# Kernel optimization log

Hardware: AMD Instinct MI355X
Metric: run time of the kernel (lower is better)

Reference implementation:

```python
import jax, jax.numpy as jnp
import numpy as np

N, F, D, O, E = 100000, 32, 3, 32, 1600000


def setup_inputs() -> dict:
    key = jax.random.key(0)
    k = jax.random.split(key, 7)
    x = jax.random.normal(k[0], (N, F), dtype=jnp.float32)
    edge_index = jax.random.randint(k[1], (2, E), 0, N, dtype=jnp.int64)
    pseudo = jax.random.uniform(k[2], (E, D), dtype=jnp.float32)
    # learned params (uniform init as in torch reset_parameters)
    bound = 1.0 / np.sqrt(F)
    mu = jax.random.uniform(k[3], (F, D), minval=-bound, maxval=bound, dtype=jnp.float32)
    sigma = jax.random.uniform(k[4], (F, D), minval=0.1, maxval=1.0, dtype=jnp.float32)
    W = jax.random.uniform(k[5], (O, F), minval=-bound, maxval=bound, dtype=jnp.float32)
    b = jax.random.uniform(k[6], (O,), minval=-bound, maxval=bound, dtype=jnp.float32)
    return {"x": x, "edge_index": edge_index, "pseudo": pseudo,
            "mu": mu, "sigma": sigma, "W": W, "b": b}


def reference(x, edge_index, pseudo, mu, sigma, W, b):
    row, col = edge_index[0], edge_index[1]
    # per-edge, per-channel gaussian mixture weight: (E,F)
    diff = pseudo[:, None, :] - mu[None, :, :]           # (E,F,D)
    logw = jnp.sum(-0.5 * diff ** 2 / (1e-14 + sigma[None] ** 2), axis=-1)
    gaussian = jnp.exp(logw)                              # (E,F)
    msg = x[col] * gaussian                               # gather + weight, (E,F)
    out = jax.ops.segment_sum(msg, row, num_segments=x.shape[0])  # scatter_add, (N,F)
    return out @ W.T + b                                  # linear, (N,O)
```

## Files before the change

kernel.cpp:

```cpp
#include <hip/hip_runtime.h>

#define N_NODES 100000
#define F_DIM   32
#define D_DIM   3
#define O_DIM   32
#define E_EDGES 1600000

#define CAP        32
#define SPILL_MAX  262144
#define NSTRIPES   512
#define EPS        (E_EDGES / NSTRIPES)


struct __align__(16) Spill { unsigned row, col, q01, q2; };

__global__ __launch_bounds__(256) void k_bucket(
        const int* __restrict__ ei, const float* __restrict__ pseudo,
        int* __restrict__ cnt, int* __restrict__ spillcnt,
        unsigned long long* __restrict__ rec, Spill* __restrict__ spill) {
    const int c    = blockIdx.x & 7;
    const int s    = blockIdx.x >> 3;
    const int base = s * EPS;
    const int end  = base + EPS;

    for (int e = base + threadIdx.x; e < end; e += 256) {
        const int row = ei[e];
        if (((row >> 12) & 7) != c) continue;
        const int   col = ei[E_EDGES + e];
        const float p0  = pseudo[e * 3 + 0];
        const float p1  = pseudo[e * 3 + 1];
        const float p2  = pseudo[e * 3 + 2];
        const int p = atomicAdd(&cnt[row], 1);
        if (p < CAP) {
            const unsigned q0 = min((unsigned)(p0 * 32768.f + 0.5f), 32767u);
            const unsigned q1 = min((unsigned)(p1 * 65536.f + 0.5f), 65535u);
            const unsigned q2 = min((unsigned)(p2 * 65536.f + 0.5f), 65535u);
            const unsigned lo = (unsigned)col | (q0 << 17);
            const unsigned hi = q1 | (q2 << 16);
            rec[(size_t)row * CAP + p] = ((unsigned long long)hi << 32) | lo;
        } else {
            const int t = atomicAdd(spillcnt, 1);
            if (t < SPILL_MAX) {
                Spill sp;
                sp.row = (unsigned)row;
                sp.col = (unsigned)col;
                sp.q01 = min((unsigned)(p0 * 65536.f + 0.5f), 65535u)
                       | (min((unsigned)(p1 * 65536.f + 0.5f), 65535u) << 16);
                sp.q2  = min((unsigned)(p2 * 65536.f + 0.5f), 65535u);
                spill[t] = sp;
            }
        }
    }
}

__global__ __launch_bounds__(128) void k_gather_linear(
        const float* __restrict__ x, const int* __restrict__ cnt,
        const unsigned long long* __restrict__ rec,
        const int* __restrict__ spillcnt, const Spill* __restrict__ spill,
        const float* __restrict__ mu, const float* __restrict__ sigma,
        const float* __restrict__ W, const float* __restrict__ b,
        float* __restrict__ out) {
    __shared__ float arow[2][F_DIM];

    const int lane = threadIdx.x & 63;
    const int wid  = threadIdx.x >> 6;
    const int f    = lane & 31;
    const int half = lane >> 5;
    const int n    = blockIdx.x * 2 + wid;

    const float m0 = mu[f * 3 + 0], m1 = mu[f * 3 + 1], m2 = mu[f * 3 + 2];
    const float s0 = sigma[f * 3 + 0], s1 = sigma[f * 3 + 1], s2 = sigma[f * 3 + 2];
    const float c0 = 0.5f / (1e-14f + s0 * s0);
    const float c1 = 0.5f / (1e-14f + s1 * s1);
    const float c2 = 0.5f / (1e-14f + s2 * s2);

    const int cn = cnt[n];
    const int m  = min(cn, CAP);
    const unsigned long long* rb = rec + (size_t)n * CAP;

    unsigned long long r[16];
#pragma unroll
    for (int k = 0; k < 16; ++k) {
        r[k] = rb[half + 2 * k];
    }

    float xv[16];
#pragma unroll
    for (int k = 0; k < 16; ++k) {
        const int col = min((int)((unsigned)r[k] & 0x1FFFFu), N_NODES - 1);
        xv[k] = x[(size_t)col * F_DIM + f];
    }

    float a0 = 0.f, a1 = 0.f;
#pragma unroll
    for (int k = 0; k < 16; ++k) {
        const int j = half + 2 * k;
        if (j < m) {
            const unsigned lo = (unsigned)r[k];
            const unsigned hi = (unsigned)(r[k] >> 32);
            const float d0 = (float)(lo >> 17) * (1.f / 32768.f) - m0;
            const float d1 = (float)(hi & 0xFFFFu) * (1.f / 65536.f) - m1;
            const float d2 = (float)(hi >> 16) * (1.f / 65536.f) - m2;
            const float g  = __expf(-(c0 * d0 * d0 + c1 * d1 * d1 + c2 * d2 * d2));
            if (k & 1) a1 += xv[k] * g; else a0 += xv[k] * g;
        }
    }

    if (cn > CAP && half == 0) {
        const int sn = min(*spillcnt, SPILL_MAX);
        for (int k = 0; k < sn; ++k) {
            const Spill sp = spill[k];
            if ((int)sp.row != n) continue;
            const float d0 = (float)(sp.q01 & 0xFFFFu) * (1.f / 65536.f) - m0;
            const float d1 = (float)(sp.q01 >> 16) * (1.f / 65536.f) - m1;
            const float d2 = (float)sp.q2 * (1.f / 65536.f) - m2;
            const float g  = __expf(-(c0 * d0 * d0 + c1 * d1 * d1 + c2 * d2 * d2));
            a0 += x[(size_t)sp.col * F_DIM + f] * g;
        }
    }

    float a = a0 + a1;
    a += __shfl_xor(a, 32, 64);
    if (half == 0) arow[wid][f] = a;
    __syncthreads();

    float w[16];
    const float* wrow = W + (size_t)f * F_DIM + half * 16;
#pragma unroll
    for (int q = 0; q < 4; ++q) {
        const float4 t = ((const float4*)wrow)[q];
        w[4 * q + 0] = t.x; w[4 * q + 1] = t.y;
        w[4 * q + 2] = t.z; w[4 * q + 3] = t.w;
    }
    const float* ar = &arow[wid][half * 16];
    float s = 0.f;
#pragma unroll
    for (int q = 0; q < 4; ++q) {
        const float4 v = ((const float4*)ar)[q];
        s += v.x * w[4 * q + 0] + v.y * w[4 * q + 1]
           + v.z * w[4 * q + 2] + v.w * w[4 * q + 3];
    }
    s += __shfl_xor(s, 32, 64);
    if (half == 0) out[(size_t)n * F_DIM + f] = s + b[f];
}

__global__ void gmm_edge_scatter(const float* __restrict__ x,
                                 const int*   __restrict__ edge_index,
                                 const float* __restrict__ pseudo,
                                 const float* __restrict__ mu,
                                 const float* __restrict__ sigma,
                                 float* __restrict__ acc) {
    const int f = threadIdx.x & 31;
    const float m0 = mu[f * 3 + 0], m1 = mu[f * 3 + 1], m2 = mu[f * 3 + 2];
    const float s0 = sigma[f * 3 + 0], s1 = sigma[f * 3 + 1], s2 = sigma[f * 3 + 2];
    const float c0 = 0.5f / (1e-14f + s0 * s0);
    const float c1 = 0.5f / (1e-14f + s1 * s1);
    const float c2 = 0.5f / (1e-14f + s2 * s2);
    int group   = (blockIdx.x * blockDim.x + threadIdx.x) >> 5;
    int ngroups = (gridDim.x * blockDim.x) >> 5;
    for (int e = group; e < E_EDGES; e += ngroups) {
        const int row = edge_index[e];
        const int col = edge_index[E_EDGES + e];
        const float p0 = pseudo[e * 3 + 0], p1 = pseudo[e * 3 + 1], p2 = pseudo[e * 3 + 2];
        const float d0 = p0 - m0, d1 = p1 - m1, d2 = p2 - m2;
        const float g  = __expf(-(c0 * d0 * d0 + c1 * d1 * d1 + c2 * d2 * d2));
        atomicAdd(&acc[(size_t)row * F_DIM + f], x[(size_t)col * F_DIM + f] * g);
    }
}

__global__ void gmm_linear2(const float* __restrict__ acc,
                            const float* __restrict__ W,
                            const float* __restrict__ b,
                            float* __restrict__ out) {
    const int o = threadIdx.x & 31;
    const int n = (blockIdx.x * blockDim.x + threadIdx.x) >> 5;
    if (n >= N_NODES) return;
    const float* wrow = W + (size_t)o * F_DIM;
    const float* ap   = acc + (size_t)n * F_DIM;
    float s = b[o];
#pragma unroll
    for (int q = 0; q < 8; ++q) {
        const float4 wv = ((const float4*)wrow)[q];
        const float4 av = ((const float4*)ap)[q];
        s += av.x * wv.x + av.y * wv.y + av.z * wv.z + av.w * wv.w;
    }
    out[(size_t)n * F_DIM + o] = s;
}

extern "C" void kernel_launch(void* const* d_in, const int* in_sizes, int n_in,
                              void* d_out, int out_size, void* d_ws, size_t ws_size,
                              hipStream_t stream) {
    const float* x          = (const float*)d_in[0];
    const int*   edge_index = (const int*)  d_in[1];
    const float* pseudo     = (const float*)d_in[2];
    const float* mu         = (const float*)d_in[3];
    const float* sigma      = (const float*)d_in[4];
    const float* W          = (const float*)d_in[5];
    const float* b          = (const float*)d_in[6];
    float*       out        = (float*)d_out;

    const size_t CNT_OFF    = 0;
    const size_t SPC_OFF    = (size_t)N_NODES * 4;
    const size_t ZERO_BYTES = SPC_OFF + 4;
    const size_t REC_OFF    = 409600;
    const size_t REC_BYTES  = (size_t)N_NODES * CAP * 8;
    const size_t SPILL_OFF  = REC_OFF + REC_BYTES;
    const size_t NEED       = SPILL_OFF + (size_t)SPILL_MAX * sizeof(Spill);

    if (ws_size >= NEED) {
        char* ws = (char*)d_ws;
        int*                cnt      = (int*)(ws + CNT_OFF);
        int*                spillcnt = (int*)(ws + SPC_OFF);
        unsigned long long* rec      = (unsigned long long*)(ws + REC_OFF);
        Spill*              spill    = (Spill*)(ws + SPILL_OFF);

        hipMemsetAsync(ws, 0, ZERO_BYTES, stream);
        k_bucket<<<8 * NSTRIPES, 256, 0, stream>>>(
            edge_index, pseudo, cnt, spillcnt, rec, spill);
        k_gather_linear<<<N_NODES / 2, 128, 0, stream>>>(
            x, cnt, rec, spillcnt, spill, mu, sigma, W, b, out);
    } else {
        float* acc = (float*)d_ws;
        hipMemsetAsync(acc, 0, (size_t)N_NODES * F_DIM * sizeof(float), stream);
        gmm_edge_scatter<<<4096, 256, 0, stream>>>(x, edge_index, pseudo, mu, sigma, acc);
        gmm_linear2<<<(N_NODES * 32 + 255) / 256, 256, 0, stream>>>(acc, W, b, out);
    }
}
```

Measured before the change: 274.3 us.

## Remap gather lanes to float2 feature pairs and loop only over actual edges

```diff
diff --git a/kernel.cpp b/kernel.cpp
--- a/kernel.cpp
+++ b/kernel.cpp
@@ -53,95 +53,121 @@
     }
 }
 
-__global__ __launch_bounds__(128) void k_gather_linear(
+__global__ __launch_bounds__(256) void k_gather_linear(
         const float* __restrict__ x, const int* __restrict__ cnt,
         const unsigned long long* __restrict__ rec,
         const int* __restrict__ spillcnt, const Spill* __restrict__ spill,
         const float* __restrict__ mu, const float* __restrict__ sigma,
         const float* __restrict__ W, const float* __restrict__ b,
         float* __restrict__ out) {
-    __shared__ float arow[2][F_DIM];
+    __shared__ float arow[4][F_DIM];
 
     const int lane = threadIdx.x & 63;
     const int wid  = threadIdx.x >> 6;
-    const int f    = lane & 31;
-    const int half = lane >> 5;
-    const int n    = blockIdx.x * 2 + wid;
-
-    const float m0 = mu[f * 3 + 0], m1 = mu[f * 3 + 1], m2 = mu[f * 3 + 2];
-    const float s0 = sigma[f * 3 + 0], s1 = sigma[f * 3 + 1], s2 = sigma[f * 3 + 2];
-    const float c0 = 0.5f / (1e-14f + s0 * s0);
-    const float c1 = 0.5f / (1e-14f + s1 * s1);
-    const float c2 = 0.5f / (1e-14f + s2 * s2);
+    const int fq   = lane & 15;
+    const int q    = lane >> 4;
+    const int f0   = 2 * fq;
+    const int n    = blockIdx.x * 4 + wid;
+
+    const float ma0 = mu[f0 * 3 + 0], ma1 = mu[f0 * 3 + 1], ma2 = mu[f0 * 3 + 2];
+    const float mb0 = mu[f0 * 3 + 3], mb1 = mu[f0 * 3 + 4], mb2 = mu[f0 * 3 + 5];
+    const float sa0 = sigma[f0 * 3 + 0], sa1 = sigma[f0 * 3 + 1], sa2 = sigma[f0 * 3 + 2];
+    const float sb0 = sigma[f0 * 3 + 3], sb1 = sigma[f0 * 3 + 4], sb2 = sigma[f0 * 3 + 5];
+    const float ca0 = 0.5f / (1e-14f + sa0 * sa0);
+    const float ca1 = 0.5f / (1e-14f + sa1 * sa1);
+    const float ca2 = 0.5f / (1e-14f + sa2 * sa2);
+    const float cb0 = 0.5f / (1e-14f + sb0 * sb0);
+    const float cb1 = 0.5f / (1e-14f + sb1 * sb1);
+    const float cb2 = 0.5f / (1e-14f + sb2 * sb2);
 
     const int cn = cnt[n];
     const int m  = min(cn, CAP);
     const unsigned long long* rb = rec + (size_t)n * CAP;
-
-    unsigned long long r[16];
-#pragma unroll
-    for (int k = 0; k < 16; ++k) {
-        r[k] = rb[half + 2 * k];
-    }
-
-    float xv[16];
-#pragma unroll
-    for (int k = 0; k < 16; ++k) {
-        const int col = min((int)((unsigned)r[k] & 0x1FFFFu), N_NODES - 1);
-        xv[k] = x[(size_t)col * F_DIM + f];
-    }
-
-    float a0 = 0.f, a1 = 0.f;
-#pragma unroll
-    for (int k = 0; k < 16; ++k) {
-        const int j = half + 2 * k;
-        if (j < m) {
-            const unsigned lo = (unsigned)r[k];
-            const unsigned hi = (unsigned)(r[k] >> 32);
-            const float d0 = (float)(lo >> 17) * (1.f / 32768.f) - m0;
-            const float d1 = (float)(hi & 0xFFFFu) * (1.f / 65536.f) - m1;
-            const float d2 = (float)(hi >> 16) * (1.f / 65536.f) - m2;
-            const float g  = __expf(-(c0 * d0 * d0 + c1 * d1 * d1 + c2 * d2 * d2));
-            if (k & 1) a1 += xv[k] * g; else a0 += xv[k] * g;
-        }
-    }
-
-    if (cn > CAP && half == 0) {
+    const float2* x2 = (const float2*)x;
+
+    float Ax0 = 0.f, Ay0 = 0.f, Ax1 = 0.f, Ay1 = 0.f;
+    int j = q;
+
+    for (; j + 4 < m; j += 8) {
+        const unsigned long long r0 = rb[j];
+        const unsigned long long r1 = rb[j + 4];
+        const unsigned lo0 = (unsigned)r0, hi0 = (unsigned)(r0 >> 32);
+        const unsigned lo1 = (unsigned)r1, hi1 = (unsigned)(r1 >> 32);
+        const float2 xv0 = x2[(size_t)(lo0 & 0x1FFFFu) * 16 + fq];
+        const float2 xv1 = x2[(size_t)(lo1 & 0x1FFFFu) * 16 + fq];
+        const float u00 = (float)(lo0 >> 17) * (1.f / 32768.f);
+        const float u01 = (float)(hi0 & 0xFFFFu) * (1.f / 65536.f);
+        const float u02 = (float)(hi0 >> 16) * (1.f / 65536.f);
+        const float u10 = (float)(lo1 >> 17) * (1.f / 32768.f);
+        const float u11 = (float)(hi1 & 0xFFFFu) * (1.f / 65536.f);
+        const float u12 = (float)(hi1 >> 16) * (1.f / 65536.f);
+        const float e0a0 = u00 - ma0, e0a1 = u01 - ma1, e0a2 = u02 - ma2;
+        const float e0b0 = u00 - mb0, e0b1 = u01 - mb1, e0b2 = u02 - mb2;
+        const float g0a = __expf(-(ca0 * e0a0 * e0a0 + ca1 * e0a1 * e0a1 + ca2 * e0a2 * e0a2));
+        const float g0b = __expf(-(cb0 * e0b0 * e0b0 + cb1 * e0b1 * e0b1 + cb2 * e0b2 * e0b2));
+        const float e1a0 = u10 - ma0, e1a1 = u11 - ma1, e1a2 = u12 - ma2;
+        const float e1b0 = u10 - mb0, e1b1 = u11 - mb1, e1b2 = u12 - mb2;
+        const float g1a = __expf(-(ca0 * e1a0 * e1a0 + ca1 * e1a1 * e1a1 + ca2 * e1a2 * e1a2));
+        const float g1b = __expf(-(cb0 * e1b0 * e1b0 + cb1 * e1b1 * e1b1 + cb2 * e1b2 * e1b2));
+        Ax0 += xv0.x * g0a;  Ay0 += xv0.y * g0b;
+        Ax1 += xv1.x * g1a;  Ay1 += xv1.y * g1b;
+    }
+    for (; j < m; j += 4) {
+        const unsigned long long r0 = rb[j];
+        const unsigned lo0 = (unsigned)r0, hi0 = (unsigned)(r0 >> 32);
+        const float2 xv0 = x2[(size_t)(lo0 & 0x1FFFFu) * 16 + fq];
+        const float u00 = (float)(lo0 >> 17) * (1.f / 32768.f);
+        const float u01 = (float)(hi0 & 0xFFFFu) * (1.f / 65536.f);
+        const float u02 = (float)(hi0 >> 16) * (1.f / 65536.f);
+        const float e0a0 = u00 - ma0, e0a1 = u01 - ma1, e0a2 = u02 - ma2;
+        const float e0b0 = u00 - mb0, e0b1 = u01 - mb1, e0b2 = u02 - mb2;
+        const float g0a = __expf(-(ca0 * e0a0 * e0a0 + ca1 * e0a1 * e0a1 + ca2 * e0a2 * e0a2));
+        const float g0b = __expf(-(cb0 * e0b0 * e0b0 + cb1 * e0b1 * e0b1 + cb2 * e0b2 * e0b2));
+        Ax0 += xv0.x * g0a;  Ay0 += xv0.y * g0b;
+    }
+
+    if (cn > CAP && q == 0) {
         const int sn = min(*spillcnt, SPILL_MAX);
         for (int k = 0; k < sn; ++k) {
             const Spill sp = spill[k];
             if ((int)sp.row != n) continue;
-            const float d0 = (float)(sp.q01 & 0xFFFFu) * (1.f / 65536.f) - m0;
-            const float d1 = (float)(sp.q01 >> 16) * (1.f / 65536.f) - m1;
-            const float d2 = (float)sp.q2 * (1.f / 65536.f) - m2;
-            const float g  = __expf(-(c0 * d0 * d0 + c1 * d1 * d1 + c2 * d2 * d2));
-            a0 += x[(size_t)sp.col * F_DIM + f] * g;
+            const float u0 = (float)(sp.q01 & 0xFFFFu) * (1.f / 65536.f);
+            const float u1 = (float)(sp.q01 >> 16) * (1.f / 65536.f);
+            const float u2 = (float)sp.q2 * (1.f / 65536.f);
+            const float da0 = u0 - ma0, da1 = u1 - ma1, da2 = u2 - ma2;
+            const float db0 = u0 - mb0, db1 = u1 - mb1, db2 = u2 - mb2;
+            const float ga = __expf(-(ca0 * da0 * da0 + ca1 * da1 * da1 + ca2 * da2 * da2));
+            const float gb = __expf(-(cb0 * db0 * db0 + cb1 * db1 * db1 + cb2 * db2 * db2));
+            const float2 xv = x2[(size_t)sp.col * 16 + fq];
+            Ax0 += xv.x * ga;  Ay0 += xv.y * gb;
         }
     }
 
-    float a = a0 + a1;
-    a += __shfl_xor(a, 32, 64);
-    if (half == 0) arow[wid][f] = a;
-    __syncthreads();
-
+    float ax = Ax0 + Ax1, ay = Ay0 + Ay1;
+    ax += __shfl_xor(ax, 16, 64);  ay += __shfl_xor(ay, 16, 64);
+    ax += __shfl_xor(ax, 32, 64);  ay += __shfl_xor(ay, 32, 64);
+    if (q == 0) { arow[wid][f0] = ax; arow[wid][f0 + 1] = ay; }
+
+    const int o    = lane & 31;
+    const int half = lane >> 5;
     float w[16];
-    const float* wrow = W + (size_t)f * F_DIM + half * 16;
+    const float* wrow = W + (size_t)o * F_DIM + half * 16;
 #pragma unroll
-    for (int q = 0; q < 4; ++q) {
-        const float4 t = ((const float4*)wrow)[q];
-        w[4 * q + 0] = t.x; w[4 * q + 1] = t.y;
-        w[4 * q + 2] = t.z; w[4 * q + 3] = t.w;
+    for (int t = 0; t < 4; ++t) {
+        const float4 v = ((const float4*)wrow)[t];
+        w[4 * t + 0] = v.x; w[4 * t + 1] = v.y;
+        w[4 * t + 2] = v.z; w[4 * t + 3] = v.w;
     }
     const float* ar = &arow[wid][half * 16];
     float s = 0.f;
 #pragma unroll
-    for (int q = 0; q < 4; ++q) {
-        const float4 v = ((const float4*)ar)[q];
-        s += v.x * w[4 * q + 0] + v.y * w[4 * q + 1]
-           + v.z * w[4 * q + 2] + v.w * w[4 * q + 3];
+    for (int t = 0; t < 4; ++t) {
+        const float4 v = ((const float4*)ar)[t];
+        s += v.x * w[4 * t + 0] + v.y * w[4 * t + 1]
+           + v.z * w[4 * t + 2] + v.w * w[4 * t + 3];
     }
     s += __shfl_xor(s, 32, 64);
-    if (half == 0) out[(size_t)n * F_DIM + f] = s + b[f];
+    if (half == 0) out[(size_t)n * F_DIM + o] = s + b[o];
 }
 
 __global__ void gmm_edge_scatter(const float* __restrict__ x,
@@ -179,9 +205,9 @@
     const float* ap   = acc + (size_t)n * F_DIM;
     float s = b[o];
 #pragma unroll
-    for (int q = 0; q < 8; ++q) {
-        const float4 wv = ((const float4*)wrow)[q];
-        const float4 av = ((const float4*)ap)[q];
+    for (int t = 0; t < 8; ++t) {
+        const float4 wv = ((const float4*)wrow)[t];
+        const float4 av = ((const float4*)ap)[t];
         s += av.x * wv.x + av.y * wv.y + av.z * wv.z + av.w * wv.w;
     }
     out[(size_t)n * F_DIM + o] = s;
@@ -217,7 +243,7 @@
         hipMemsetAsync(ws, 0, ZERO_BYTES, stream);
         k_bucket<<<8 * NSTRIPES, 256, 0, stream>>>(
             edge_index, pseudo, cnt, spillcnt, rec, spill);
-        k_gather_linear<<<N_NODES / 2, 128, 0, stream>>>(
+        k_gather_linear<<<N_NODES / 4, 256, 0, stream>>>(
             x, cnt, rec, spillcnt, spill, mu, sigma, W, b, out);
     } else {
         float* acc = (float*)d_ws;
```

After: 262.5 us. 1.05x faster.
